# Performance work log

Measured on AMD Instinct MI355X. Metric: run time of the kernel, lower is better.

## Reference

```python
import jax, jax.numpy as jnp
import numpy as np

TOP_K = 2

def setup_inputs() -> dict:
    key = jax.random.key(0)
    k0, k1, k2 = jax.random.split(key, 3)
    N, D, E = 32768, 1024, 8  # tokens, in_dim, expert_num
    x = jax.random.normal(k0, (N, D), dtype=jnp.float32)
    W1 = jax.random.normal(k1, (D // 2, D), dtype=jnp.float32) * (1.0 / np.sqrt(D))
    b1 = jnp.zeros((D // 2,), dtype=jnp.float32)
    W2 = jax.random.normal(k2, (E, D // 2), dtype=jnp.float32) * (1.0 / np.sqrt(D // 2))
    b2 = jnp.zeros((E,), dtype=jnp.float32)
    return {"x": x, "W1": W1, "b1": b1, "W2": W2, "b2": b2}

def reference(x, W1, b1, W2, b2):
    E = W2.shape[0]
    # gate: two stacked Linears (no nonlinearity between, as in source)
    h = x @ W1.T + b1                      # [N, D/2]
    router_logits = h @ W2.T + b2          # [N, E]
    router_probs = jax.nn.softmax(router_logits, axis=-1)
    router_weights, top_k_indices = jax.lax.top_k(router_probs, TOP_K)  # [N, K]
    router_weights = router_weights / jnp.sum(router_weights, axis=-1, keepdims=True)
    expert_masks = jax.nn.one_hot(top_k_indices, E, dtype=jnp.int32)   # [N, K, E]
    expert_masks = jnp.transpose(expert_masks, (2, 1, 0))              # [E, K, N]
    return (router_logits, router_weights, top_k_indices, expert_masks)
```

## Files before the change

kernel.cpp:

```cpp
#include <hip/hip_runtime.h>
#include <math.h>


#define N_TOK 32768
#define D_IN  1024
#define D_H   512
#define N_EXP 8

#define BM      128
#define THREADS 512
#define NKT2    32
#define WSLOTS  (64 * 1024)

typedef _Float16 f16;
typedef __attribute__((ext_vector_type(4)))  _Float16 f16x4;
typedef __attribute__((ext_vector_type(8)))  _Float16 f16x8;
typedef __attribute__((ext_vector_type(16))) float    f32x16;

#define MFMA(a, b, c) __builtin_amdgcn_mfma_f32_32x32x16_f16((a), (b), (c), 0, 0, 0)

__global__ void split_w1(const float* __restrict__ W1,
                         f16* __restrict__ wsH, f16* __restrict__ wsL) {
    const int s = blockIdx.x * 256 + threadIdx.x;
    const int kt  = s >> 10;
    const int ctg = (s >> 6) & 15;
    const int l   = s & 63;
    const int n   = ctg * 32 + (l & 31);
    const int k   = kt * 16 + (l >> 5) * 8;
    const float* src = &W1[(size_t)n * D_IN + k];
    float4 a0 = *(const float4*)src;
    float4 a1 = *(const float4*)(src + 4);
    f16x8 hi, lo;
#pragma unroll
    for (int j = 0; j < 4; ++j) {
        float v0 = ((const float*)&a0)[j];
        float v1 = ((const float*)&a1)[j];
        _Float16 h0 = (_Float16)v0, h1 = (_Float16)v1;
        hi[j] = h0;     hi[j + 4] = h1;
        lo[j] = (_Float16)(v0 - (float)h0);
        lo[j + 4] = (_Float16)(v1 - (float)h1);
    }
    *(f16x8*)&wsH[(size_t)s * 8] = hi;
    *(f16x8*)&wsL[(size_t)s * 8] = lo;
}

__global__ __launch_bounds__(THREADS, 1)
void moe_router_mfma(const float* __restrict__ x,
                     const f16* __restrict__ wH,
                     const f16* __restrict__ wL,
                     const float* __restrict__ b1,
                     const float* __restrict__ W2,
                     const float* __restrict__ b2,
                     float* __restrict__ out)
{
    __shared__ __align__(16) unsigned char SMEM[65536];
    __shared__ __align__(16) float W2s[N_EXP * D_H];
    __shared__ __align__(16) float b1s[D_H];
    __shared__ float b2s[N_EXP];

    f16*   AS  = (f16*)SMEM;
    float* h_s = (float*)SMEM;

    const int t    = threadIdx.x;
    const int w    = t >> 6;
    const int lane = t & 63;
    const int m0   = blockIdx.x * BM;

    f32x16 a0c0 = {}, a0c1 = {}, a1c0 = {}, a1c1 = {};
    f32x16 a2c0 = {}, a2c1 = {}, a3c0 = {}, a3c1 = {};

    const int fA   = t >> 1;
    const int qA   = t & 1;
    const int rowA = (fA >> 6) * 32 + (fA & 31);
    const int kA   = ((fA >> 5) & 1) * 8 + qA * 4;
    const float* xsrc = x + (size_t)(m0 + rowA) * D_IN + kA;
    const int aDst = fA * 8 + qA * 4;

    const size_t bOff0 = (size_t)(2 * w + 0) * 512 + (size_t)lane * 8;
    const size_t bOff1 = (size_t)(2 * w + 1) * 512 + (size_t)lane * 8;

    auto stageAwrite = [&](const float4& xv, int buf, int sub) {
        f16x4 hi, lo;
        float v[4] = {xv.x, xv.y, xv.z, xv.w};
#pragma unroll
        for (int j = 0; j < 4; ++j) {
            _Float16 h = (_Float16)v[j];
            hi[j] = h;
            lo[j] = (_Float16)(v[j] - (float)h);
        }
        *(f16x4*)&AS[(buf * 2 + 0) * 4096 + sub * 2048 + aDst] = hi;
        *(f16x4*)&AS[(buf * 2 + 1) * 4096 + sub * 2048 + aDst] = lo;
    };

    {
        float4 xv0 = *(const float4*)xsrc;
        float4 xv1 = *(const float4*)(xsrc + 16);
        stageAwrite(xv0, 0, 0);
        stageAwrite(xv1, 0, 1);
    }
    __syncthreads();

    for (int ktt = 0; ktt < NKT2; ++ktt) {
        const int cur = ktt & 1;
        const int nxt = cur ^ 1;
        const size_t kb0 = (size_t)(2 * ktt) * 8192;
        const size_t kb1 = (size_t)(2 * ktt + 1) * 8192;

        f16x8 B0h0 = *(const f16x8*)(wH + kb0 + bOff0);
        f16x8 B0h1 = *(const f16x8*)(wH + kb0 + bOff1);
        f16x8 B0l0 = *(const f16x8*)(wL + kb0 + bOff0);
        f16x8 B0l1 = *(const f16x8*)(wL + kb0 + bOff1);
        f16x8 B1h0 = *(const f16x8*)(wH + kb1 + bOff0);
        f16x8 B1h1 = *(const f16x8*)(wH + kb1 + bOff1);
        f16x8 B1l0 = *(const f16x8*)(wL + kb1 + bOff0);
        f16x8 B1l1 = *(const f16x8*)(wL + kb1 + bOff1);
        float4 xn0 = {0.f, 0.f, 0.f, 0.f}, xn1 = {0.f, 0.f, 0.f, 0.f};
        if (ktt + 1 < NKT2) {
            xn0 = *(const float4*)(xsrc + (size_t)(ktt + 1) * 32);
            xn1 = *(const float4*)(xsrc + (size_t)(ktt + 1) * 32 + 16);
        }

        const f16* ah = &AS[(cur * 2 + 0) * 4096];
        const f16* al = &AS[(cur * 2 + 1) * 4096];

        {
            f16x8 ah0 = *(const f16x8*)&ah[(0 * 64 + lane) * 8];
            f16x8 al0 = *(const f16x8*)&al[(0 * 64 + lane) * 8];
            f16x8 ah1 = *(const f16x8*)&ah[(1 * 64 + lane) * 8];
            f16x8 al1 = *(const f16x8*)&al[(1 * 64 + lane) * 8];
            f16x8 ah2 = *(const f16x8*)&ah[(2 * 64 + lane) * 8];
            f16x8 al2 = *(const f16x8*)&al[(2 * 64 + lane) * 8];
            f16x8 ah3 = *(const f16x8*)&ah[(3 * 64 + lane) * 8];
            f16x8 al3 = *(const f16x8*)&al[(3 * 64 + lane) * 8];
            __builtin_amdgcn_s_setprio(1);
            a0c0 = MFMA(ah0, B0h0, a0c0); a0c0 = MFMA(al0, B0h0, a0c0); a0c0 = MFMA(ah0, B0l0, a0c0);
            a1c0 = MFMA(ah1, B0h0, a1c0); a1c0 = MFMA(al1, B0h0, a1c0); a1c0 = MFMA(ah1, B0l0, a1c0);
            a2c0 = MFMA(ah2, B0h0, a2c0); a2c0 = MFMA(al2, B0h0, a2c0); a2c0 = MFMA(ah2, B0l0, a2c0);
            a3c0 = MFMA(ah3, B0h0, a3c0); a3c0 = MFMA(al3, B0h0, a3c0); a3c0 = MFMA(ah3, B0l0, a3c0);
            a0c1 = MFMA(ah0, B0h1, a0c1); a0c1 = MFMA(al0, B0h1, a0c1); a0c1 = MFMA(ah0, B0l1, a0c1);
            a1c1 = MFMA(ah1, B0h1, a1c1); a1c1 = MFMA(al1, B0h1, a1c1); a1c1 = MFMA(ah1, B0l1, a1c1);
            a2c1 = MFMA(ah2, B0h1, a2c1); a2c1 = MFMA(al2, B0h1, a2c1); a2c1 = MFMA(ah2, B0l1, a2c1);
            a3c1 = MFMA(ah3, B0h1, a3c1); a3c1 = MFMA(al3, B0h1, a3c1); a3c1 = MFMA(ah3, B0l1, a3c1);
            __builtin_amdgcn_s_setprio(0);
        }
        {
            f16x8 ah0 = *(const f16x8*)&ah[2048 + (0 * 64 + lane) * 8];
            f16x8 al0 = *(const f16x8*)&al[2048 + (0 * 64 + lane) * 8];
            f16x8 ah1 = *(const f16x8*)&ah[2048 + (1 * 64 + lane) * 8];
            f16x8 al1 = *(const f16x8*)&al[2048 + (1 * 64 + lane) * 8];
            f16x8 ah2 = *(const f16x8*)&ah[2048 + (2 * 64 + lane) * 8];
            f16x8 al2 = *(const f16x8*)&al[2048 + (2 * 64 + lane) * 8];
            f16x8 ah3 = *(const f16x8*)&ah[2048 + (3 * 64 + lane) * 8];
            f16x8 al3 = *(const f16x8*)&al[2048 + (3 * 64 + lane) * 8];
            __builtin_amdgcn_s_setprio(1);
            a0c0 = MFMA(ah0, B1h0, a0c0); a0c0 = MFMA(al0, B1h0, a0c0); a0c0 = MFMA(ah0, B1l0, a0c0);
            a1c0 = MFMA(ah1, B1h0, a1c0); a1c0 = MFMA(al1, B1h0, a1c0); a1c0 = MFMA(ah1, B1l0, a1c0);
            a2c0 = MFMA(ah2, B1h0, a2c0); a2c0 = MFMA(al2, B1h0, a2c0); a2c0 = MFMA(ah2, B1l0, a2c0);
            a3c0 = MFMA(ah3, B1h0, a3c0); a3c0 = MFMA(al3, B1h0, a3c0); a3c0 = MFMA(ah3, B1l0, a3c0);
            a0c1 = MFMA(ah0, B1h1, a0c1); a0c1 = MFMA(al0, B1h1, a0c1); a0c1 = MFMA(ah0, B1l1, a0c1);
            a1c1 = MFMA(ah1, B1h1, a1c1); a1c1 = MFMA(al1, B1h1, a1c1); a1c1 = MFMA(ah1, B1l1, a1c1);
            a2c1 = MFMA(ah2, B1h1, a2c1); a2c1 = MFMA(al2, B1h1, a2c1); a2c1 = MFMA(ah2, B1l1, a2c1);
            a3c1 = MFMA(ah3, B1h1, a3c1); a3c1 = MFMA(al3, B1h1, a3c1); a3c1 = MFMA(ah3, B1l1, a3c1);
            __builtin_amdgcn_s_setprio(0);
        }

        if (ktt + 1 < NKT2) {
            stageAwrite(xn0, nxt, 0);
            stageAwrite(xn1, nxt, 1);
        }
        __syncthreads();
    }

    ((float4*)W2s)[t * 2]     = ((const float4*)W2)[t * 2];
    ((float4*)W2s)[t * 2 + 1] = ((const float4*)W2)[t * 2 + 1];
    if (t < D_H / 4) ((float4*)b1s)[t] = ((const float4*)b1)[t];
    if (t < N_EXP) b2s[t] = b2[t];
    __syncthreads();

    const int n0  = w * 64 + (lane & 31);
    const int n1  = n0 + 32;
    const float bn0 = b1s[n0];
    const float bn1 = b1s[n1];

    float* out_logits = out;
    float* out_w      = out + (size_t)N_TOK * N_EXP;
    float* out_i      = out_w + (size_t)N_TOK * 2;
    float* out_m      = out_i + (size_t)N_TOK * 2;

    auto reduce_rows = [&](int rt) {
#pragma unroll
        for (int rr2 = 0; rr2 < 4; ++rr2) {
            const int rl   = w * 4 + rr2;
            const int grow = m0 + rt * 32 + rl;
            float4 ha = *(const float4*)&h_s[rl * 512 + lane * 4];
            float4 hb = *(const float4*)&h_s[rl * 512 + 256 + lane * 4];
            float v1 = -3.4e38f, v2 = -3.4e38f;
            int   i1 = 0, i2 = 0;
            float pls[8];
#pragma unroll
            for (int e = 0; e < N_EXP; ++e) {
                float4 wa = *(const float4*)&W2s[e * D_H + lane * 4];
                float4 wb = *(const float4*)&W2s[e * D_H + 256 + lane * 4];
                float s = ha.x * wa.x;
                s = fmaf(ha.y, wa.y, s);
                s = fmaf(ha.z, wa.z, s);
                s = fmaf(ha.w, wa.w, s);
                s = fmaf(hb.x, wb.x, s);
                s = fmaf(hb.y, wb.y, s);
                s = fmaf(hb.z, wb.z, s);
                s = fmaf(hb.w, wb.w, s);
#pragma unroll
                for (int off = 1; off < 64; off <<= 1)
                    s += __shfl_xor(s, off);
                s += b2s[e];
                pls[e] = s;
                if (s > v1)      { v2 = v1; i2 = i1; v1 = s; i1 = e; }
                else if (s > v2) { v2 = s;  i2 = e; }
            }
            const float rr   = expf(v2 - v1);
            const float wden = 1.f / (1.f + rr);
            if (lane == 0) {
                float4 lo4 = {pls[0], pls[1], pls[2], pls[3]};
                float4 hi4 = {pls[4], pls[5], pls[6], pls[7]};
                *(float4*)&out_logits[(size_t)grow * N_EXP]     = lo4;
                *(float4*)&out_logits[(size_t)grow * N_EXP + 4] = hi4;
                float2 wv = {wden, rr * wden};
                *(float2*)&out_w[(size_t)grow * 2] = wv;
                float2 iv = {(float)i1, (float)i2};
                *(float2*)&out_i[(size_t)grow * 2] = iv;
            }
            if (lane < 16) {
                const int e   = lane >> 1;
                const int kk  = lane & 1;
                const int sel = kk ? i2 : i1;
                out_m[((size_t)(e * 2 + kk)) * N_TOK + grow] = (sel == e) ? 1.0f : 0.0f;
            }
        }
    };

#define DO_GROUP(AC0, AC1, RT) do {                                            \
        _Pragma("unroll")                                                      \
        for (int rr = 0; rr < 16; ++rr) {                                      \
            const int rl = (rr & 3) + 8 * (rr >> 2) + 4 * (lane >> 5);         \
            h_s[rl * 512 + n0] = AC0[rr] + bn0;                                \
            h_s[rl * 512 + n1] = AC1[rr] + bn1;                                \
        }                                                                      \
        __syncthreads();                                                       \
        reduce_rows(RT);                                                       \
        __syncthreads();                                                       \
    } while (0)

    DO_GROUP(a0c0, a0c1, 0);
    DO_GROUP(a1c0, a1c1, 1);
    DO_GROUP(a2c0, a2c1, 2);
    DO_GROUP(a3c0, a3c1, 3);
#undef DO_GROUP
}

extern "C" void kernel_launch(void* const* d_in, const int* in_sizes, int n_in,
                              void* d_out, int out_size, void* d_ws, size_t ws_size,
                              hipStream_t stream) {
    const float* x  = (const float*)d_in[0];
    const float* W1 = (const float*)d_in[1];
    const float* b1 = (const float*)d_in[2];
    const float* W2 = (const float*)d_in[3];
    const float* b2 = (const float*)d_in[4];
    float* out = (float*)d_out;

    f16* wsH = (f16*)d_ws;
    f16* wsL = wsH + (size_t)WSLOTS * 8;

    split_w1<<<WSLOTS / 256, 256, 0, stream>>>(W1, wsH, wsL);
    moe_router_mfma<<<N_TOK / BM, THREADS, 0, stream>>>(x, wsH, wsL, b1, W2, b2, out);
}
```

Before: 133.0 us.

## Split block row tiles across 16 waves to halve per-wave accumulators

Doubles the workgroup to 1024 threads, with waves split into two row groups of 64 rows and eight column groups. Each wave now holds four accumulator tiles instead of eight, and the x staging and W2 load are spread over twice the threads. The MFMA issue order is interleaved across independent accumulators. This is meant to raise latency hiding and cut register pressure, at the cost of each B fragment being loaded by twice as many waves and of more waves per barrier.

```diff
diff --git a/kernel.cpp b/kernel.cpp
--- a/kernel.cpp
+++ b/kernel.cpp
@@ -8,7 +8,7 @@
 #define N_EXP 8
 
 #define BM      128
-#define THREADS 512
+#define THREADS 1024
 #define NKT2    32
 #define WSLOTS  (64 * 1024)
 
@@ -64,22 +64,26 @@
     const int t    = threadIdx.x;
     const int w    = t >> 6;
     const int lane = t & 63;
+    const int rg   = w >> 3;
+    const int cg   = w & 7;
     const int m0   = blockIdx.x * BM;
 
     f32x16 a0c0 = {}, a0c1 = {}, a1c0 = {}, a1c1 = {};
-    f32x16 a2c0 = {}, a2c1 = {}, a3c0 = {}, a3c1 = {};
-
-    const int fA   = t >> 1;
-    const int qA   = t & 1;
-    const int rowA = (fA >> 6) * 32 + (fA & 31);
-    const int kA   = ((fA >> 5) & 1) * 8 + qA * 4;
-    const float* xsrc = x + (size_t)(m0 + rowA) * D_IN + kA;
-    const int aDst = fA * 8 + qA * 4;
-
-    const size_t bOff0 = (size_t)(2 * w + 0) * 512 + (size_t)lane * 8;
-    const size_t bOff1 = (size_t)(2 * w + 1) * 512 + (size_t)lane * 8;
-
-    auto stageAwrite = [&](const float4& xv, int buf, int sub) {
+
+    const int subA = t >> 9;
+    const int t9   = t & 511;
+    const int fA   = t9 >> 1;
+    const int qA   = t9 & 1;
+    const int lA   = fA & 63;
+    const int rowA = (fA >> 6) * 32 + (lA & 31);
+    const int kA   = ((lA >> 5) & 1) * 8 + qA * 4;
+    const float* xsrc = x + (size_t)(m0 + rowA) * D_IN + subA * 16 + kA;
+    const int aDst = subA * 2048 + fA * 8 + qA * 4;
+
+    const size_t bOff0 = (size_t)(2 * cg + 0) * 512 + (size_t)lane * 8;
+    const size_t bOff1 = (size_t)(2 * cg + 1) * 512 + (size_t)lane * 8;
+
+    auto stageAwrite = [&](const float4& xv, int buf) {
         f16x4 hi, lo;
         float v[4] = {xv.x, xv.y, xv.z, xv.w};
 #pragma unroll
@@ -88,96 +92,63 @@
             hi[j] = h;
             lo[j] = (_Float16)(v[j] - (float)h);
         }
-        *(f16x4*)&AS[(buf * 2 + 0) * 4096 + sub * 2048 + aDst] = hi;
-        *(f16x4*)&AS[(buf * 2 + 1) * 4096 + sub * 2048 + aDst] = lo;
+        *(f16x4*)&AS[(buf * 2 + 0) * 4096 + aDst] = hi;
+        *(f16x4*)&AS[(buf * 2 + 1) * 4096 + aDst] = lo;
     };
 
-    {
-        float4 xv0 = *(const float4*)xsrc;
-        float4 xv1 = *(const float4*)(xsrc + 16);
-        stageAwrite(xv0, 0, 0);
-        stageAwrite(xv1, 0, 1);
-    }
+    stageAwrite(*(const float4*)xsrc, 0);
     __syncthreads();
 
     for (int ktt = 0; ktt < NKT2; ++ktt) {
         const int cur = ktt & 1;
         const int nxt = cur ^ 1;
-        const size_t kb0 = (size_t)(2 * ktt) * 8192;
-        const size_t kb1 = (size_t)(2 * ktt + 1) * 8192;
-
-        f16x8 B0h0 = *(const f16x8*)(wH + kb0 + bOff0);
-        f16x8 B0h1 = *(const f16x8*)(wH + kb0 + bOff1);
-        f16x8 B0l0 = *(const f16x8*)(wL + kb0 + bOff0);
-        f16x8 B0l1 = *(const f16x8*)(wL + kb0 + bOff1);
-        f16x8 B1h0 = *(const f16x8*)(wH + kb1 + bOff0);
-        f16x8 B1h1 = *(const f16x8*)(wH + kb1 + bOff1);
-        f16x8 B1l0 = *(const f16x8*)(wL + kb1 + bOff0);
-        f16x8 B1l1 = *(const f16x8*)(wL + kb1 + bOff1);
-        float4 xn0 = {0.f, 0.f, 0.f, 0.f}, xn1 = {0.f, 0.f, 0.f, 0.f};
-        if (ktt + 1 < NKT2) {
-            xn0 = *(const float4*)(xsrc + (size_t)(ktt + 1) * 32);
-            xn1 = *(const float4*)(xsrc + (size_t)(ktt + 1) * 32 + 16);
-        }
+
+        float4 xn = {0.f, 0.f, 0.f, 0.f};
+        if (ktt + 1 < NKT2)
+            xn = *(const float4*)(xsrc + (size_t)(ktt + 1) * 32);
 
         const f16* ah = &AS[(cur * 2 + 0) * 4096];
         const f16* al = &AS[(cur * 2 + 1) * 4096];
 
-        {
-            f16x8 ah0 = *(const f16x8*)&ah[(0 * 64 + lane) * 8];
-            f16x8 al0 = *(const f16x8*)&al[(0 * 64 + lane) * 8];
-            f16x8 ah1 = *(const f16x8*)&ah[(1 * 64 + lane) * 8];
-            f16x8 al1 = *(const f16x8*)&al[(1 * 64 + lane) * 8];
-            f16x8 ah2 = *(const f16x8*)&ah[(2 * 64 + lane) * 8];
-            f16x8 al2 = *(const f16x8*)&al[(2 * 64 + lane) * 8];
-            f16x8 ah3 = *(const f16x8*)&ah[(3 * 64 + lane) * 8];
-            f16x8 al3 = *(const f16x8*)&al[(3 * 64 + lane) * 8];
+#pragma unroll
+        for (int sub = 0; sub < 2; ++sub) {
+            const size_t kb = (size_t)(2 * ktt + sub) * 8192;
+            f16x8 Bh0 = *(const f16x8*)(wH + kb + bOff0);
+            f16x8 Bh1 = *(const f16x8*)(wH + kb + bOff1);
+            f16x8 Bl0 = *(const f16x8*)(wL + kb + bOff0);
+            f16x8 Bl1 = *(const f16x8*)(wL + kb + bOff1);
+            const int sb = sub * 2048;
+            f16x8 ah0 = *(const f16x8*)&ah[sb + ((rg * 2 + 0) * 64 + lane) * 8];
+            f16x8 al0 = *(const f16x8*)&al[sb + ((rg * 2 + 0) * 64 + lane) * 8];
+            f16x8 ah1 = *(const f16x8*)&ah[sb + ((rg * 2 + 1) * 64 + lane) * 8];
+            f16x8 al1 = *(const f16x8*)&al[sb + ((rg * 2 + 1) * 64 + lane) * 8];
+
             __builtin_amdgcn_s_setprio(1);
-            a0c0 = MFMA(ah0, B0h0, a0c0); a0c0 = MFMA(al0, B0h0, a0c0); a0c0 = MFMA(ah0, B0l0, a0c0);
-            a1c0 = MFMA(ah1, B0h0, a1c0); a1c0 = MFMA(al1, B0h0, a1c0); a1c0 = MFMA(ah1, B0l0, a1c0);
-            a2c0 = MFMA(ah2, B0h0, a2c0); a2c0 = MFMA(al2, B0h0, a2c0); a2c0 = MFMA(ah2, B0l0, a2c0);
-            a3c0 = MFMA(ah3, B0h0, a3c0); a3c0 = MFMA(al3, B0h0, a3c0); a3c0 = MFMA(ah3, B0l0, a3c0);
-            a0c1 = MFMA(ah0, B0h1, a0c1); a0c1 = MFMA(al0, B0h1, a0c1); a0c1 = MFMA(ah0, B0l1, a0c1);
-            a1c1 = MFMA(ah1, B0h1, a1c1); a1c1 = MFMA(al1, B0h1, a1c1); a1c1 = MFMA(ah1, B0l1, a1c1);
-            a2c1 = MFMA(ah2, B0h1, a2c1); a2c1 = MFMA(al2, B0h1, a2c1); a2c1 = MFMA(ah2, B0l1, a2c1);
-            a3c1 = MFMA(ah3, B0h1, a3c1); a3c1 = MFMA(al3, B0h1, a3c1); a3c1 = MFMA(ah3, B0l1, a3c1);
+            a0c0 = MFMA(ah0, Bh0, a0c0);
+            a1c0 = MFMA(ah1, Bh0, a1c0);
+            a0c1 = MFMA(ah0, Bh1, a0c1);
+            a1c1 = MFMA(ah1, Bh1, a1c1);
+            a0c0 = MFMA(al0, Bh0, a0c0);
+            a1c0 = MFMA(al1, Bh0, a1c0);
+            a0c1 = MFMA(al0, Bh1, a0c1);
+            a1c1 = MFMA(al1, Bh1, a1c1);
+            a0c0 = MFMA(ah0, Bl0, a0c0);
+            a1c0 = MFMA(ah1, Bl0, a1c0);
+            a0c1 = MFMA(ah0, Bl1, a0c1);
+            a1c1 = MFMA(ah1, Bl1, a1c1);
             __builtin_amdgcn_s_setprio(0);
         }
-        {
-            f16x8 ah0 = *(const f16x8*)&ah[2048 + (0 * 64 + lane) * 8];
-            f16x8 al0 = *(const f16x8*)&al[2048 + (0 * 64 + lane) * 8];
-            f16x8 ah1 = *(const f16x8*)&ah[2048 + (1 * 64 + lane) * 8];
-            f16x8 al1 = *(const f16x8*)&al[2048 + (1 * 64 + lane) * 8];
-            f16x8 ah2 = *(const f16x8*)&ah[2048 + (2 * 64 + lane) * 8];
-            f16x8 al2 = *(const f16x8*)&al[2048 + (2 * 64 + lane) * 8];
-            f16x8 ah3 = *(const f16x8*)&ah[2048 + (3 * 64 + lane) * 8];
-            f16x8 al3 = *(const f16x8*)&al[2048 + (3 * 64 + lane) * 8];
-            __builtin_amdgcn_s_setprio(1);
-            a0c0 = MFMA(ah0, B1h0, a0c0); a0c0 = MFMA(al0, B1h0, a0c0); a0c0 = MFMA(ah0, B1l0, a0c0);
-            a1c0 = MFMA(ah1, B1h0, a1c0); a1c0 = MFMA(al1, B1h0, a1c0); a1c0 = MFMA(ah1, B1l0, a1c0);
-            a2c0 = MFMA(ah2, B1h0, a2c0); a2c0 = MFMA(al2, B1h0, a2c0); a2c0 = MFMA(ah2, B1l0, a2c0);
-            a3c0 = MFMA(ah3, B1h0, a3c0); a3c0 = MFMA(al3, B1h0, a3c0); a3c0 = MFMA(ah3, B1l0, a3c0);
-            a0c1 = MFMA(ah0, B1h1, a0c1); a0c1 = MFMA(al0, B1h1, a0c1); a0c1 = MFMA(ah0, B1l1, a0c1);
-            a1c1 = MFMA(ah1, B1h1, a1c1); a1c1 = MFMA(al1, B1h1, a1c1); a1c1 = MFMA(ah1, B1l1, a1c1);
-            a2c1 = MFMA(ah2, B1h1, a2c1); a2c1 = MFMA(al2, B1h1, a2c1); a2c1 = MFMA(ah2, B1l1, a2c1);
-            a3c1 = MFMA(ah3, B1h1, a3c1); a3c1 = MFMA(al3, B1h1, a3c1); a3c1 = MFMA(ah3, B1l1, a3c1);
-            __builtin_amdgcn_s_setprio(0);
-        }
-
-        if (ktt + 1 < NKT2) {
-            stageAwrite(xn0, nxt, 0);
-            stageAwrite(xn1, nxt, 1);
-        }
+
+        if (ktt + 1 < NKT2) stageAwrite(xn, nxt);
         __syncthreads();
     }
 
-    ((float4*)W2s)[t * 2]     = ((const float4*)W2)[t * 2];
-    ((float4*)W2s)[t * 2 + 1] = ((const float4*)W2)[t * 2 + 1];
+    ((float4*)W2s)[t] = ((const float4*)W2)[t];
     if (t < D_H / 4) ((float4*)b1s)[t] = ((const float4*)b1)[t];
     if (t < N_EXP) b2s[t] = b2[t];
     __syncthreads();
 
-    const int n0  = w * 64 + (lane & 31);
+    const int n0  = cg * 64 + (lane & 31);
     const int n1  = n0 + 32;
     const float bn0 = b1s[n0];
     const float bn1 = b1s[n1];
@@ -187,11 +158,11 @@
     float* out_i      = out_w + (size_t)N_TOK * 2;
     float* out_m      = out_i + (size_t)N_TOK * 2;
 
-    auto reduce_rows = [&](int rt) {
-#pragma unroll
-        for (int rr2 = 0; rr2 < 4; ++rr2) {
-            const int rl   = w * 4 + rr2;
-            const int grow = m0 + rt * 32 + rl;
+    auto reduce_rows = [&](int g) {
+#pragma unroll
+        for (int rr2 = 0; rr2 < 2; ++rr2) {
+            const int rl   = w * 2 + rr2;
+            const int grow = m0 + g * 32 + rl;
             float4 ha = *(const float4*)&h_s[rl * 512 + lane * 4];
             float4 hb = *(const float4*)&h_s[rl * 512 + 256 + lane * 4];
             float v1 = -3.4e38f, v2 = -3.4e38f;
@@ -238,22 +209,24 @@
         }
     };
 
-#define DO_GROUP(AC0, AC1, RT) do {                                            \
-        _Pragma("unroll")                                                      \
-        for (int rr = 0; rr < 16; ++rr) {                                      \
-            const int rl = (rr & 3) + 8 * (rr >> 2) + 4 * (lane >> 5);         \
-            h_s[rl * 512 + n0] = AC0[rr] + bn0;                                \
-            h_s[rl * 512 + n1] = AC1[rr] + bn1;                                \
+#define DO_GROUP(RGSEL, AC0, AC1, G) do {                                      \
+        if (rg == (RGSEL)) {                                                   \
+            _Pragma("unroll")                                                  \
+            for (int rr = 0; rr < 16; ++rr) {                                  \
+                const int rl = (rr & 3) + 8 * (rr >> 2) + 4 * (lane >> 5);     \
+                h_s[rl * 512 + n0] = AC0[rr] + bn0;                            \
+                h_s[rl * 512 + n1] = AC1[rr] + bn1;                            \
+            }                                                                  \
         }                                                                      \
         __syncthreads();                                                       \
-        reduce_rows(RT);                                                       \
+        reduce_rows(G);                                                        \
         __syncthreads();                                                       \
     } while (0)
 
-    DO_GROUP(a0c0, a0c1, 0);
-    DO_GROUP(a1c0, a1c1, 1);
-    DO_GROUP(a2c0, a2c1, 2);
-    DO_GROUP(a3c0, a3c1, 3);
+    DO_GROUP(0, a0c0, a0c1, 0);
+    DO_GROUP(0, a1c0, a1c1, 1);
+    DO_GROUP(1, a0c0, a0c1, 2);
+    DO_GROUP(1, a1c0, a1c1, 3);
 #undef DO_GROUP
 }
 
```

Result: slower. 150.8 us (+13.4%).
